# Kernel optimization log

Hardware: AMD Instinct MI355X
Metric: run time of the kernel (lower is better)

Reference implementation:

```python
import jax, jax.numpy as jnp
import numpy as np
from jax import lax

EPS = 1e-08

def _sobel_edges(x, sx, sy):
    # x: [B, C, H, W]; depthwise 3x3 conv per channel, SAME padding.
    B, C, H, W = x.shape
    kx = jnp.tile(sx, (C, 1, 1, 1))  # [C,1,3,3] OIHW with feature_group_count=C
    ky = jnp.tile(sy, (C, 1, 1, 1))
    dn = ('NCHW', 'OIHW', 'NCHW')
    gx = lax.conv_general_dilated(x, kx, (1, 1), 'SAME',
                                  dimension_numbers=dn, feature_group_count=C)
    gy = lax.conv_general_dilated(x, ky, (1, 1), 'SAME',
                                  dimension_numbers=dn, feature_group_count=C)
    return jnp.sqrt(gx * gx + gy * gy + EPS)

def setup_inputs() -> dict:
    key = jax.random.key(0)
    k1, k2 = jax.random.split(key)
    B, C, H, W = 16, 8, 512, 512
    source_latent = jax.random.normal(k1, (B, C, H, W), dtype=jnp.float32)
    edited_latent = jax.random.normal(k2, (B, C, H, W), dtype=jnp.float32)
    sx = jnp.array([[-1., 0., 1.], [-2., 0., 2.], [-1., 0., 1.]], dtype=jnp.float32).reshape(1, 1, 3, 3)
    sy = jnp.array([[-1., -2., -1.], [0., 0., 0.], [1., 2., 1.]], dtype=jnp.float32).reshape(1, 1, 3, 3)
    return {"source_latent": source_latent, "edited_latent": edited_latent, "sx": sx, "sy": sy}

def reference(source_latent, edited_latent, sx, sy):
    e_src = _sobel_edges(source_latent, sx, sy)
    e_edit = _sobel_edges(edited_latent, sx, sy)
    diff = e_edit - e_src
    return jnp.mean(diff * diff)
```

## Files before the change

### kernel.cpp

```cpp
#include <hip/hip_runtime.h>


#define EPS 1e-8f

constexpr int W_DIM  = 512;
constexpr int H_DIM  = 512;
constexpr int NIMG   = 128;
constexpr int ROWS   = 32;
constexpr int CHUNKS = H_DIM / ROWS;
constexpr int TPB    = 128;
constexpr int NBLK   = NIMG * CHUNKS;
constexpr double TOTAL_ELEMS = 33554432.0;

__global__ __launch_bounds__(TPB) void edge_loss_stage1(
    const float* __restrict__ src, const float* __restrict__ edt,
    float* __restrict__ partial)
{
    const int blk   = blockIdx.x;
    const int n     = blk / CHUNKS;
    const int chunk = blk % CHUNKS;
    const int r0    = chunk * ROWS;
    const float* sbase = src + (size_t)n * H_DIM * W_DIM;
    const float* ebase = edt + (size_t)n * H_DIM * W_DIM;
    const int c0 = threadIdx.x * 4;

    float sa0[4], sa1[4], sa2[4], sb0[4], sb1[4], sb2[4];
    float ea0[4], ea1[4], ea2[4], eb0[4], eb1[4], eb2[4];

    auto loadrow = [&](const float* base, int h, float* a, float* b) {
        if (h < 0 || h >= H_DIM) {
            #pragma unroll
            for (int i = 0; i < 4; ++i) { a[i] = 0.f; b[i] = 0.f; }
            return;
        }
        const float* row = base + (size_t)h * W_DIM;
        float4 v = *reinterpret_cast<const float4*>(row + c0);
        float xl = (c0 > 0)          ? row[c0 - 1] : 0.f;
        float xr = (c0 + 4 < W_DIM)  ? row[c0 + 4] : 0.f;
        float p0 = xl,  p1 = v.x, p2 = v.y, p3 = v.z, p4 = v.w, p5 = xr;
        a[0] = p2 - p0;  b[0] = p0 + 2.f*p1 + p2;
        a[1] = p3 - p1;  b[1] = p1 + 2.f*p2 + p3;
        a[2] = p4 - p2;  b[2] = p2 + 2.f*p3 + p4;
        a[3] = p5 - p3;  b[3] = p3 + 2.f*p4 + p5;
    };

    loadrow(sbase, r0 - 1, sa0, sb0);
    loadrow(ebase, r0 - 1, ea0, eb0);
    loadrow(sbase, r0,     sa1, sb1);
    loadrow(ebase, r0,     ea1, eb1);

    float acc = 0.f;
    for (int h = r0; h < r0 + ROWS; ++h) {
        loadrow(sbase, h + 1, sa2, sb2);
        loadrow(ebase, h + 1, ea2, eb2);
        #pragma unroll
        for (int i = 0; i < 4; ++i) {
            float sgx = sa0[i] + 2.f*sa1[i] + sa2[i];
            float sgy = sb2[i] - sb0[i];
            float es  = __builtin_amdgcn_sqrtf(sgx*sgx + sgy*sgy + EPS);
            float egx = ea0[i] + 2.f*ea1[i] + ea2[i];
            float egy = eb2[i] - eb0[i];
            float ee  = __builtin_amdgcn_sqrtf(egx*egx + egy*egy + EPS);
            float d   = ee - es;
            acc += d * d;
        }
        #pragma unroll
        for (int i = 0; i < 4; ++i) {
            sa0[i] = sa1[i]; sa1[i] = sa2[i];
            sb0[i] = sb1[i]; sb1[i] = sb2[i];
            ea0[i] = ea1[i]; ea1[i] = ea2[i];
            eb0[i] = eb1[i]; eb1[i] = eb2[i];
        }
    }

    #pragma unroll
    for (int off = 32; off > 0; off >>= 1)
        acc += __shfl_down(acc, off);
    __shared__ float wsum[TPB / 64];
    const int wid  = threadIdx.x >> 6;
    const int lane = threadIdx.x & 63;
    if (lane == 0) wsum[wid] = acc;
    __syncthreads();
    if (threadIdx.x == 0) {
        float tot = 0.f;
        #pragma unroll
        for (int i = 0; i < TPB / 64; ++i) tot += wsum[i];
        partial[blk] = tot;
    }
}

__global__ __launch_bounds__(256) void edge_loss_stage2(
    const float* __restrict__ partial, float* __restrict__ out, int nparts)
{
    double acc = 0.0;
    for (int i = threadIdx.x; i < nparts; i += 256)
        acc += (double)partial[i];
    #pragma unroll
    for (int off = 32; off > 0; off >>= 1)
        acc += __shfl_down(acc, off);
    __shared__ double wsum[4];
    const int wid  = threadIdx.x >> 6;
    const int lane = threadIdx.x & 63;
    if (lane == 0) wsum[wid] = acc;
    __syncthreads();
    if (threadIdx.x == 0) {
        double t = 0.0;
        #pragma unroll
        for (int i = 0; i < 4; ++i) t += wsum[i];
        out[0] = (float)(t / TOTAL_ELEMS);
    }
}

extern "C" void kernel_launch(void* const* d_in, const int* in_sizes, int n_in,
                              void* d_out, int out_size, void* d_ws, size_t ws_size,
                              hipStream_t stream) {
    const float* src = (const float*)d_in[0];
    const float* edt = (const float*)d_in[1];
    float* out     = (float*)d_out;
    float* partial = (float*)d_ws;

    edge_loss_stage1<<<dim3(NBLK), dim3(TPB), 0, stream>>>(src, edt, partial);
    edge_loss_stage2<<<dim3(1), dim3(256), 0, stream>>>(partial, out, NBLK);
}
```

Baseline: 53.27 us.

## Prefetch rows two ahead, get halos via lane shuffles, reuse row sums

Restructures the row loop into a software pipeline with four row buffers, so global loads for rows h+2..h+5 are issued before earlier rows are consumed. Horizontal halo values now come from wave shuffles instead of extra scalar global loads. Only the seam lanes between the two waves load one extra element. The vertical Sobel combination is carried as running partial sums with FMAs to cut ALU work. The cost is more registers and more complex boundary handling at the last row.

```diff
diff --git a/kernel.cpp b/kernel.cpp
--- a/kernel.cpp
+++ b/kernel.cpp
@@ -12,74 +12,142 @@
 constexpr int NBLK   = NIMG * CHUNKS;
 constexpr double TOTAL_ELEMS = 33554432.0;
 
+struct RowBuf { float4 s, e; float ss, es; };
+
 __global__ __launch_bounds__(TPB) void edge_loss_stage1(
     const float* __restrict__ src, const float* __restrict__ edt,
     float* __restrict__ partial)
 {
-    const int blk   = blockIdx.x;
-    const int n     = blk / CHUNKS;
-    const int chunk = blk % CHUNKS;
-    const int r0    = chunk * ROWS;
-    const float* sbase = src + (size_t)n * H_DIM * W_DIM;
-    const float* ebase = edt + (size_t)n * H_DIM * W_DIM;
-    const int c0 = threadIdx.x * 4;
+    const int blk  = blockIdx.x;
+    const int img  = blk / CHUNKS;
+    const int r0   = (blk % CHUNKS) * ROWS;
+    const int wv   = threadIdx.x >> 6;
+    const int lane = threadIdx.x & 63;
+    const int c0   = threadIdx.x * 4;
 
-    float sa0[4], sa1[4], sa2[4], sb0[4], sb1[4], sb2[4];
-    float ea0[4], ea1[4], ea2[4], eb0[4], eb1[4], eb2[4];
+    const float* simg = src + (size_t)img * (H_DIM * W_DIM);
+    const float* eimg = edt + (size_t)img * (H_DIM * W_DIM);
 
-    auto loadrow = [&](const float* base, int h, float* a, float* b) {
-        if (h < 0 || h >= H_DIM) {
-            #pragma unroll
-            for (int i = 0; i < 4; ++i) { a[i] = 0.f; b[i] = 0.f; }
-            return;
-        }
-        const float* row = base + (size_t)h * W_DIM;
-        float4 v = *reinterpret_cast<const float4*>(row + c0);
-        float xl = (c0 > 0)          ? row[c0 - 1] : 0.f;
-        float xr = (c0 + 4 < W_DIM)  ? row[c0 + 4] : 0.f;
-        float p0 = xl,  p1 = v.x, p2 = v.y, p3 = v.z, p4 = v.w, p5 = xr;
-        a[0] = p2 - p0;  b[0] = p0 + 2.f*p1 + p2;
-        a[1] = p3 - p1;  b[1] = p1 + 2.f*p2 + p3;
-        a[2] = p4 - p2;  b[2] = p2 + 2.f*p3 + p4;
-        a[3] = p5 - p3;  b[3] = p3 + 2.f*p4 + p5;
+    const bool seam_active = (wv == 0) ? (lane == 63) : (lane == 0);
+    const int  seamcol     = (wv == 0) ? 256 : 255;
+
+    float sP0[4], sP1[4], sQ0[4], sQ1[4];
+    float eP0[4], eP1[4], eQ0[4], eQ1[4];
+    float acc = 0.f;
+
+    auto issue = [&](int h, RowBuf& rb) {
+        int hc = h < 0 ? 0 : (h >= H_DIM ? H_DIM - 1 : h);
+        const float* srow = simg + (size_t)hc * W_DIM;
+        const float* erow = eimg + (size_t)hc * W_DIM;
+        rb.s = *reinterpret_cast<const float4*>(srow + c0);
+        rb.e = *reinterpret_cast<const float4*>(erow + c0);
+        rb.ss = 0.f; rb.es = 0.f;
+        if (seam_active) { rb.ss = srow[seamcol]; rb.es = erow[seamcol]; }
     };
 
-    loadrow(sbase, r0 - 1, sa0, sb0);
-    loadrow(ebase, r0 - 1, ea0, eb0);
-    loadrow(sbase, r0,     sa1, sb1);
-    loadrow(ebase, r0,     ea1, eb1);
+    auto halos = [&](const RowBuf& rb, float sp[6], float ep[6]) {
+        float slT = __shfl_up(rb.s.w, 1);
+        float srT = __shfl_down(rb.s.x, 1);
+        float elT = __shfl_up(rb.e.w, 1);
+        float erT = __shfl_down(rb.e.x, 1);
+        sp[0] = (lane == 0)  ? rb.ss : slT;
+        sp[5] = (lane == 63) ? rb.ss : srT;
+        ep[0] = (lane == 0)  ? rb.es : elT;
+        ep[5] = (lane == 63) ? rb.es : erT;
+        sp[1]=rb.s.x; sp[2]=rb.s.y; sp[3]=rb.s.z; sp[4]=rb.s.w;
+        ep[1]=rb.e.x; ep[2]=rb.e.y; ep[3]=rb.e.z; ep[4]=rb.e.w;
+    };
 
-    float acc = 0.f;
-    for (int h = r0; h < r0 + ROWS; ++h) {
-        loadrow(sbase, h + 1, sa2, sb2);
-        loadrow(ebase, h + 1, ea2, eb2);
+    auto consume = [&](const RowBuf& rb, int h) {
+        if (h < H_DIM) {
+            float sp[6], ep[6];
+            halos(rb, sp, ep);
+            #pragma unroll
+            for (int i = 0; i < 4; ++i) {
+                float a  = sp[i+2] - sp[i];
+                float b  = sp[i] + 2.f*sp[i+1] + sp[i+2];
+                float gx = sP0[i] + a;
+                float gy = b - sQ0[i];
+                sP0[i] = fmaf(2.f, a, sP1[i]); sP1[i] = a;
+                sQ0[i] = sQ1[i]; sQ1[i] = b;
+                float es = __builtin_amdgcn_sqrtf(fmaf(gx, gx, fmaf(gy, gy, EPS)));
+                float a2  = ep[i+2] - ep[i];
+                float b2  = ep[i] + 2.f*ep[i+1] + ep[i+2];
+                float gx2 = eP0[i] + a2;
+                float gy2 = b2 - eQ0[i];
+                eP0[i] = fmaf(2.f, a2, eP1[i]); eP1[i] = a2;
+                eQ0[i] = eQ1[i]; eQ1[i] = b2;
+                float ee = __builtin_amdgcn_sqrtf(fmaf(gx2, gx2, fmaf(gy2, gy2, EPS)));
+                float d = ee - es;
+                acc = fmaf(d, d, acc);
+            }
+        } else {
+            #pragma unroll
+            for (int i = 0; i < 4; ++i) {
+                float gx = sP0[i], gy = -sQ0[i];
+                sP0[i] = sP1[i]; sP1[i] = 0.f; sQ0[i] = sQ1[i]; sQ1[i] = 0.f;
+                float es = __builtin_amdgcn_sqrtf(fmaf(gx, gx, fmaf(gy, gy, EPS)));
+                float gx2 = eP0[i], gy2 = -eQ0[i];
+                eP0[i] = eP1[i]; eP1[i] = 0.f; eQ0[i] = eQ1[i]; eQ1[i] = 0.f;
+                float ee = __builtin_amdgcn_sqrtf(fmaf(gx2, gx2, fmaf(gy2, gy2, EPS)));
+                float d = ee - es;
+                acc = fmaf(d, d, acc);
+            }
+        }
+    };
+
+    RowBuf bA0, bA1, bB0, bB1;
+    issue(r0 - 1, bA0);
+    issue(r0,     bA1);
+    issue(r0 + 1, bB0);
+    issue(r0 + 2, bB1);
+
+    if (r0 > 0) {
+        float sp[6], ep[6];
+        halos(bA0, sp, ep);
         #pragma unroll
         for (int i = 0; i < 4; ++i) {
-            float sgx = sa0[i] + 2.f*sa1[i] + sa2[i];
-            float sgy = sb2[i] - sb0[i];
-            float es  = __builtin_amdgcn_sqrtf(sgx*sgx + sgy*sgy + EPS);
-            float egx = ea0[i] + 2.f*ea1[i] + ea2[i];
-            float egy = eb2[i] - eb0[i];
-            float ee  = __builtin_amdgcn_sqrtf(egx*egx + egy*egy + EPS);
-            float d   = ee - es;
-            acc += d * d;
+            sP0[i] = sp[i+2] - sp[i];
+            sQ0[i] = sp[i] + 2.f*sp[i+1] + sp[i+2];
+            eP0[i] = ep[i+2] - ep[i];
+            eQ0[i] = ep[i] + 2.f*ep[i+1] + ep[i+2];
         }
+    } else {
+        #pragma unroll
+        for (int i = 0; i < 4; ++i) { sP0[i]=0.f; sQ0[i]=0.f; eP0[i]=0.f; eQ0[i]=0.f; }
+    }
+    {
+        float sp[6], ep[6];
+        halos(bA1, sp, ep);
         #pragma unroll
         for (int i = 0; i < 4; ++i) {
-            sa0[i] = sa1[i]; sa1[i] = sa2[i];
-            sb0[i] = sb1[i]; sb1[i] = sb2[i];
-            ea0[i] = ea1[i]; ea1[i] = ea2[i];
-            eb0[i] = eb1[i]; eb1[i] = eb2[i];
+            float a  = sp[i+2] - sp[i];
+            sP0[i] = fmaf(2.f, a, sP0[i]); sP1[i] = a;
+            sQ1[i] = sp[i] + 2.f*sp[i+1] + sp[i+2];
+            float a2 = ep[i+2] - ep[i];
+            eP0[i] = fmaf(2.f, a2, eP0[i]); eP1[i] = a2;
+            eQ1[i] = ep[i] + 2.f*ep[i+1] + ep[i+2];
         }
+    }
+
+    int h = r0 + 1;
+    #pragma unroll 1
+    for (int k = 0; k < ROWS / 4; ++k, h += 4) {
+        if (h + 2 <= r0 + ROWS) issue(h + 2, bA0);
+        if (h + 3 <= r0 + ROWS) issue(h + 3, bA1);
+        consume(bB0, h);
+        consume(bB1, h + 1);
+        if (h + 4 <= r0 + ROWS) issue(h + 4, bB0);
+        if (h + 5 <= r0 + ROWS) issue(h + 5, bB1);
+        consume(bA0, h + 2);
+        consume(bA1, h + 3);
     }
 
     #pragma unroll
     for (int off = 32; off > 0; off >>= 1)
         acc += __shfl_down(acc, off);
     __shared__ float wsum[TPB / 64];
-    const int wid  = threadIdx.x >> 6;
-    const int lane = threadIdx.x & 63;
-    if (lane == 0) wsum[wid] = acc;
+    if (lane == 0) wsum[wv] = acc;
     __syncthreads();
     if (threadIdx.x == 0) {
         float tot = 0.f;
```

Result: faster. 50.88 us (-4.5%).
